# Kernel optimization log

Measured on AMD Instinct MI355X. Metric: run time of the kernel, lower is better.

## Reference

```python
import jax, jax.numpy as jnp
import numpy as np

# Config constants from init_kwargs
DIM_GROUPS = [32, 32]   # hyper_cuts_dim_groups (sum == lsh_key_dim == d_key)
K_MAX = 64              # max candidates kept per query token


def _group_exact_match(qb, kb):
    """qb, kb: [B, L, d] binary {0,1} floats.
    Returns eq[b, i, j] = True iff all d bits of query i equal key j.
    Faithful to merge(Wu-Manber prefix match, Trie full-stride match):
    the Trie stores the full binary vector chunked by stride, so a Trie hit
    requires exact equality of the whole group's bit vector, which subsumes
    the Wu-Manber prefix condition; their intersection is exact equality.
    """
    # number of mismatching bits between query i and key j
    mism = (jnp.einsum('bid,bjd->bij', qb, 1.0 - kb)
            + jnp.einsum('bid,bjd->bij', 1.0 - qb, kb))
    return mism == 0.0


def setup_inputs() -> dict:
    key = jax.random.key(0)
    k1, k2 = jax.random.split(key)
    B, L, D = 4, 2048, 64
    return {
        'query_up': jax.random.normal(k1, (B, L, D), dtype=jnp.float32),
        'key_up': jax.random.normal(k2, (B, L, D), dtype=jnp.float32),
        'head_idx': 0,
    }


def reference(query_up, key_up, head_idx):
    B, L, _ = query_up.shape
    # binary_quantize: (x > 0).float()
    qb = (query_up > 0).astype(jnp.float32)
    kb = (key_up > 0).astype(jnp.float32)
    # per dim-group exact match (Wu-Manber \cap Trie), union across groups
    match = jnp.zeros((B, L, L), dtype=bool)
    start = 0
    for gd in DIM_GROUPS:
        match = match | _group_exact_match(qb[..., start:start + gd],
                                           kb[..., start:start + gd])
        start += gd
    # gather up to K_MAX smallest matching key indices per query, pad with -1
    idx = jnp.where(match, jnp.arange(L, dtype=jnp.int32)[None, None, :], L)
    cand = jnp.sort(idx, axis=-1)[..., :K_MAX]          # [B, L, K_MAX]
    return jnp.where(cand == L, -1, cand)
```

## Files before the change

kernel.cpp:

```cpp
#include <hip/hip_runtime.h>
#include <stdint.h>


#define LSEQ 2048
#define DDIM 64
#define KMAX 64
#define QPB  32
#define NW   16
#define GROUP 16

__global__ __launch_bounds__(1024) void fused_kernel(
    const float* __restrict__ query, const float* __restrict__ key,
    int* __restrict__ out, int swizzle) {
    __shared__ uint2 ks[LSEQ];

    const int bpb = LSEQ / QPB;
    int b, qblk;
    if (swizzle) {
        int x = blockIdx.x & 7, i = blockIdx.x >> 3;
        b    = x >> 1;
        qblk = i * 2 + (x & 1);
    } else {
        b    = blockIdx.x / bpb;
        qblk = blockIdx.x % bpb;
    }
    int lane = threadIdx.x & 63;
    int wave = threadIdx.x >> 6;

    const float* qb = query + ((size_t)b * LSEQ + (size_t)qblk * QPB) * DDIM;
    int q0 = wave * 2;
    float qv0 = qb[(size_t)q0 * DDIM + lane];
    float qv1 = qb[(size_t)(q0 + 1) * DDIM + lane];
    unsigned long long qm0 = __ballot(qv0 > 0.0f);
    unsigned long long qm1 = __ballot(qv1 > 0.0f);

    const float* kb = key + (size_t)b * LSEQ * DDIM;
    for (int g = 0; g < LSEQ / (NW * GROUP); ++g) {
        float v[GROUP];
#pragma unroll
        for (int u = 0; u < GROUP; ++u)
            v[u] = kb[(size_t)(g * (NW * GROUP) + u * NW + wave) * DDIM + lane];
        unsigned long long m[GROUP];
#pragma unroll
        for (int u = 0; u < GROUP; ++u)
            m[u] = __ballot(v[u] > 0.0f);
        if (lane == 0) {
#pragma unroll
            for (int u = 0; u < GROUP; ++u)
                ks[g * (NW * GROUP) + u * NW + wave] =
                    make_uint2((unsigned)m[u], (unsigned)(m[u] >> 32));
        }
    }
    __syncthreads();

    const uint4* kt4 = (const uint4*)ks;
    unsigned long long below = (1ull << lane) - 1ull;
    for (int t = 0; t < 2; ++t) {
        unsigned long long qm = t ? qm1 : qm0;
        unsigned qa = (unsigned)qm, qg = (unsigned)(qm >> 32);
        int* ob = out + ((size_t)b * LSEQ + (size_t)qblk * QPB + q0 + t) * KMAX;

        unsigned long long acc = 0;
        int cnt = 0;
#pragma unroll
        for (int i = 0; i < LSEQ / 128; ++i) {
            uint4 kv = kt4[i * 64 + lane];
            bool mA = (kv.x == qa) | (kv.y == qg);
            bool mB = (kv.z == qa) | (kv.w == qg);
            unsigned long long s;
            s = __ballot(mA); acc |= s; cnt += __popcll(s);
            s = __ballot(mB); acc |= s; cnt += __popcll(s);
        }

        if (acc != 0) {
            int c2 = 0;
            for (int c = 0; c < LSEQ / 64; ++c) {
                uint2 kv = ks[c * 64 + lane];
                bool m = (kv.x == qa) || (kv.y == qg);
                unsigned long long mask = __ballot(m);
                if (m) {
                    int pos = c2 + __popcll(mask & below);
                    if (pos < KMAX) ob[pos] = c * 64 + lane;
                }
                c2 += __popcll(mask);
            }
        }
        if (lane >= cnt) ob[lane] = -1;
    }
}

extern "C" void kernel_launch(void* const* d_in, const int* in_sizes, int n_in,
                              void* d_out, int out_size, void* d_ws, size_t ws_size,
                              hipStream_t stream) {
    const float* q = (const float*)d_in[0];
    const float* k = (const float*)d_in[1];
    int* out = (int*)d_out;

    int total = in_sizes[0];
    int B = total / (LSEQ * DDIM);

    int grid = B * (LSEQ / QPB);
    int swizzle = (B == 4 && grid == 256) ? 1 : 0;
    fused_kernel<<<grid, 1024, 0, stream>>>(q, k, out, swizzle);
}
```

Baseline: 73.68 us.

## Claim work tiles dynamically through atomic slots, preferring the batch on the local XCD

Replaces the static block-index swizzle with dynamic work claiming. Thread 0 of each block reads its XCC id and scans a slot array in the workspace, using atomicCAS to claim a free (batch, query-block) tile, starting with the batch assigned to its XCD. The goal is for all blocks on one XCD to work on the same batch's key data, improving L2 locality. The cost is a serial scan of atomic loads at block start. The slots are never reset, so later calls may find every slot taken and fall back to the plain blockIdx mapping after two full scans.

```diff
diff --git a/kernel.cpp b/kernel.cpp
--- a/kernel.cpp
+++ b/kernel.cpp
@@ -8,24 +8,57 @@
 #define QPB  32
 #define NW   16
 #define GROUP 16
+#define MAGIC 0x13572468u
+#define XCC_ID_IMM (((4 - 1) << 11) | 20)
 
 __global__ __launch_bounds__(1024) void fused_kernel(
     const float* __restrict__ query, const float* __restrict__ key,
-    int* __restrict__ out, int swizzle) {
+    int* __restrict__ out, unsigned* __restrict__ slots, int use_claim) {
     __shared__ uint2 ks[LSEQ];
+    __shared__ int got_sh;
 
     const int bpb = LSEQ / QPB;
+    int lane = threadIdx.x & 63;
+    int wave = threadIdx.x >> 6;
+
     int b, qblk;
-    if (swizzle) {
-        int x = blockIdx.x & 7, i = blockIdx.x >> 3;
-        b    = x >> 1;
-        qblk = i * 2 + (x & 1);
+    if (use_claim) {
+        if (threadIdx.x == 0) {
+            int xcd  = __builtin_amdgcn_s_getreg(XCC_ID_IMM) & 7;
+            int pref = xcd >> 1;
+            int got = -1, stale_scans = 0;
+            while (got < 0) {
+                bool saw_free = false;
+                for (int pass = 0; pass < 4 && got < 0; ++pass) {
+                    int bb = (pref + pass) & 3;
+                    unsigned s0 = (blockIdx.x >> 3) & 63;
+                    for (int j = 0; j < 64; ++j) {
+                        unsigned idx = bb * 64 + ((s0 + j) & 63);
+                        unsigned v = __hip_atomic_load(
+                            &slots[idx], __ATOMIC_RELAXED,
+                            __HIP_MEMORY_SCOPE_AGENT);
+                        if (v != MAGIC) {
+                            saw_free = true;
+                            if (atomicCAS(&slots[idx], v, MAGIC) == v) {
+                                got = (int)idx;
+                                break;
+                            }
+                        }
+                    }
+                }
+                if (got < 0 && !saw_free) {
+                    if (++stale_scans >= 2) got = (int)blockIdx.x;
+                }
+            }
+            got_sh = got;
+        }
+        __syncthreads();
+        b    = got_sh >> 6;
+        qblk = got_sh & 63;
     } else {
         b    = blockIdx.x / bpb;
         qblk = blockIdx.x % bpb;
     }
-    int lane = threadIdx.x & 63;
-    int wave = threadIdx.x >> 6;
 
     const float* qb = query + ((size_t)b * LSEQ + (size_t)qblk * QPB) * DDIM;
     int q0 = wave * 2;
@@ -100,6 +133,8 @@
     int B = total / (LSEQ * DDIM);
 
     int grid = B * (LSEQ / QPB);
-    int swizzle = (B == 4 && grid == 256) ? 1 : 0;
-    fused_kernel<<<grid, 1024, 0, stream>>>(q, k, out, swizzle);
+    unsigned* slots = (unsigned*)d_ws;
+    int use_claim = (B == 4 && grid == 256 &&
+                     ws_size >= 256 * sizeof(unsigned)) ? 1 : 0;
+    fused_kernel<<<grid, 1024, 0, stream>>>(q, k, out, slots, use_claim);
 }
```

Measured after the change: 96.68 us. 1.31x slower.
